# Performance work log

Hardware: AMD Instinct MI355X
Metric: run time of the kernel (lower is better)

Reference implementation:

```python
import jax, jax.numpy as jnp
import numpy as np

N_QUBITS = 8
DIM = 1 << N_QUBITS  # 256
PI = float(np.pi)

# Computational-basis bit signs: s_i = +1 for bit 0, -1 for bit 1 (Z eigenvalues).
# PennyLane convention: wire 0 is the most-significant bit.
_bits = (np.arange(DIM)[:, None] >> (N_QUBITS - 1 - np.arange(N_QUBITS))[None, :]) & 1
SIGNS = jnp.asarray(1.0 - 2.0 * _bits, dtype=jnp.float32)  # [DIM, 8]
PAIR_SIGNS = SIGNS[:, :-1] * SIGNS[:, 1:]                  # [DIM, 7]


def _mlp(x, W1, b1, W2, b2, W3, b3):
    h = jax.nn.relu(x @ W1.T + b1)
    h = jax.nn.relu(h @ W2.T + b2)
    return h @ W3.T + b3


def _embed_state(x):
    """QuantumEmbedding1 (ZZ feature map, IQP-style) on |0>^8.

    H on every wire, RZ(x_i) on wire i, then for i in 0..6:
    CNOT(i,i+1); RZ((pi-x_i)(pi-x_{i+1}), wire i+1); CNOT(i,i+1).
    The whole post-Hadamard circuit is diagonal, so the statevector has
    closed form: psi_b = 2^{-4} exp(-i/2 * phi(b)).
    x: [B, 8] -> psi: [B, 256] complex64.
    """
    single = x @ SIGNS.T                                    # [B, DIM]
    zz = (PI - x[:, :-1]) * (PI - x[:, 1:])                 # [B, 7]
    phase = single + zz @ PAIR_SIGNS.T                      # [B, DIM]
    return jnp.exp(-0.5j * phase) / 16.0                    # complex64


def _mean_rho(psi):
    B = psi.shape[0]
    return jnp.einsum('bi,bj->ij', psi, jnp.conj(psi)) / B  # [256, 256]


def setup_inputs() -> dict:
    key = jax.random.key(0)
    ks = jax.random.split(key, 8)
    B = 65536
    inp = {
        'x1': jax.random.normal(ks[0], (B, 8), dtype=jnp.float32),
        'x0': jax.random.normal(ks[1], (B, 8), dtype=jnp.float32),
        'W1': jax.random.normal(ks[2], (10, 8), dtype=jnp.float32) / np.sqrt(8.0),
        'b1': jnp.zeros((10,), dtype=jnp.float32),
        'W2': jax.random.normal(ks[3], (10, 10), dtype=jnp.float32) / np.sqrt(10.0),
        'b2': jnp.zeros((10,), dtype=jnp.float32),
        'W3': jax.random.normal(ks[4], (8, 10), dtype=jnp.float32) / np.sqrt(10.0),
        'b3': jnp.zeros((8,), dtype=jnp.float32),
    }
    return inp


def reference(x1, x0, W1, b1, W2, b2, W3, b3):
    h1 = _mlp(x1, W1, b1, W2, b2, W3, b3)
    h0 = _mlp(x0, W1, b1, W2, b2, W3, b3)
    rho1 = _mean_rho(_embed_state(h1))
    rho0 = _mean_rho(_embed_state(h0))
    rho_diff = rho1 - rho0
    rho_diff = 0.5 * (rho_diff + jnp.conj(rho_diff.T))  # exact Hermitian
    eigvals = jnp.linalg.eigvalsh(rho_diff)             # real eigenvalues
    return -0.5 * jnp.sum(jnp.abs(eigvals))
```

## Files before the change

kernel.cpp:

```cpp
#include <hip/hip_runtime.h>
#include <cstdint>
#include <cstddef>
#include <utility>

#define PI_F 3.14159265358979323846f

typedef __attribute__((ext_vector_type(8))) _Float16 half8;
typedef __attribute__((ext_vector_type(4))) float f32x4;

struct U4 { unsigned int w[4]; };

static __device__ __forceinline__ unsigned int packhalf2(float c, float s) {
  _Float16 hc = (_Float16)c, hs = (_Float16)s;
  unsigned short uc = __builtin_bit_cast(unsigned short, hc);
  unsigned short us = __builtin_bit_cast(unsigned short, hs);
  return (unsigned int)uc | ((unsigned int)us << 16);
}

__global__ __launch_bounds__(256) void k_mlp(
    const float* __restrict__ x1, const float* __restrict__ x0,
    const float* __restrict__ W1, const float* __restrict__ b1,
    const float* __restrict__ W2, const float* __restrict__ b2,
    const float* __restrict__ W3, const float* __restrict__ b3,
    float* __restrict__ hz, int B, float* __restrict__ scalars,
    float* __restrict__ out) {
  int s = blockIdx.x * blockDim.x + threadIdx.x;
  if (blockIdx.x == 0 && threadIdx.x == 0) {
    scalars[0] = 0.f;
    scalars[1] = 0.f;
    out[0] = 0.f;
  }
  if (s >= 2 * B) return;
  const float* xp = (s < B) ? (x1 + (size_t)s * 8) : (x0 + (size_t)(s - B) * 8);
  float x[8];
#pragma unroll
  for (int k = 0; k < 8; k++) x[k] = xp[k];
  float a1[10];
#pragma unroll
  for (int o = 0; o < 10; o++) {
    float v = b1[o];
#pragma unroll
    for (int k = 0; k < 8; k++) v = fmaf(W1[o * 8 + k], x[k], v);
    a1[o] = fmaxf(v, 0.f);
  }
  float a2[10];
#pragma unroll
  for (int o = 0; o < 10; o++) {
    float v = b2[o];
#pragma unroll
    for (int k = 0; k < 10; k++) v = fmaf(W2[o * 10 + k], a1[k], v);
    a2[o] = fmaxf(v, 0.f);
  }
  float h[8];
#pragma unroll
  for (int o = 0; o < 8; o++) {
    float v = b3[o];
#pragma unroll
    for (int k = 0; k < 10; k++) v = fmaf(W3[o * 10 + k], a2[k], v);
    h[o] = v;
  }
  float outv[16];
#pragma unroll
  for (int k = 0; k < 8; k++) outv[k] = h[k];
#pragma unroll
  for (int k = 0; k < 7; k++) outv[8 + k] = (PI_F - h[k]) * (PI_F - h[k + 1]);
  outv[15] = 0.f;
  float4* dst = (float4*)(hz + (size_t)s * 16);
#pragma unroll
  for (int q = 0; q < 4; q++) dst[q] = ((float4*)outv)[q];
}

__global__ __launch_bounds__(512) void k_gemm_f(const float* __restrict__ hz,
                                                float* __restrict__ P) {
  __shared__ _Float16 lds[2][16384];
  __shared__ float hzb[2][32][17];
  int b = blockIdx.x;
  int qt = (b < 128) ? 0 : (b < 384 ? 1 : 2);
  int z = b - ((qt == 0) ? 0 : (qt == 1) ? 128 : 384);
  int kbPer = (qt == 1) ? 16 : 32;
  int kb0 = z * kbPer;
  int rowLocalBase = (qt == 2) ? 128 : 0;
  int bRowBase = (qt == 1) ? 128 : 0;
  int t = threadIdx.x, wave = t >> 6, lane = t & 63;
  unsigned int reMask = (kb0 < 2048) ? 0u : 0x80008000u;
  unsigned int imMask = (kb0 < 2048) ? 0x80000000u : 0x00008000u;

  int s = t & 31, octH = t >> 5;
  int oct = octH & 7, jHalf = octH >> 3;
  const int nJ = (qt == 1) ? 16 : 8;
  const int jj0 = (qt == 1) ? jHalf * 16 : ((qt == 2) ? 16 : 0) + jHalf * 8;
  const int halfoff = (2 * s) ^ (oct << 3);
  const float S5 = (oct & 4) ? -1.f : 1.f;
  const float S6 = (oct & 2) ? -1.f : 1.f;
  const float S7 = (oct & 1) ? -1.f : 1.f;

  auto loadHz = [&](int kb) {
    if (t < 128) {
      int smp = t >> 2, q = t & 3;
      const float4 v =
          *(const float4*)(hz + (size_t)(kb * 32 + smp) * 16 + q * 4);
      float* d = &hzb[kb & 1][smp][q * 4];
      d[0] = v.x;
      d[1] = v.y;
      d[2] = v.z;
      d[3] = v.w;
    }
  };

  auto gen = [&](int kb, int buf) {
    int hb = kb & 1;
    float h[8], z7[7];
#pragma unroll
    for (int k = 0; k < 8; k++) h[k] = hzb[hb][s][k];
#pragma unroll
    for (int k = 0; k < 7; k++) z7[k] = hzb[hb][s][8 + k];
    int g0 = jj0 ^ (jj0 >> 1);
    float sg[5];
#pragma unroll
    for (int w = 0; w < 5; w++) sg[w] = ((g0 >> (4 - w)) & 1) ? -1.f : 1.f;
    float phi = sg[0] * h[0] + sg[1] * h[1] + sg[2] * h[2] + sg[3] * h[3] +
                sg[4] * h[4] + S5 * h[5] + S6 * h[6] + S7 * h[7] +
                sg[0] * sg[1] * z7[0] + sg[1] * sg[2] * z7[1] +
                sg[2] * sg[3] * z7[2] + sg[3] * sg[4] * z7[3] +
                sg[4] * S5 * z7[4] + S5 * S6 * z7[5] + S6 * S7 * z7[6];
    int g = g0;
    auto emitRow = [&](int gg, float ph) {
      int lr = gg * 8 + oct - rowLocalBase;
      float r = ph * 0.07957747154594767f;
      r = r - floorf(r);
      float sv = __builtin_amdgcn_sinf(r);
      float cv = __builtin_amdgcn_cosf(r);
      *(unsigned int*)&lds[buf][lr * 64 + halfoff] = packhalf2(cv, sv);
    };
    emitRow(g, phi);
#pragma unroll
    for (int stp = 1; stp < 16; stp++) {
      if (stp >= nJ) break;
      const int bbit = __builtin_ctz(stp);
      const int w = 4 - bbit;
      float nbl = (w == 0) ? 0.f : sg[w - 1] * z7[w - 1];
      float nbr = (w == 4) ? S5 * z7[4] : sg[w + 1] * z7[w];
      phi -= 2.f * sg[w] * (h[w] + nbl + nbr);
      sg[w] = -sg[w];
      g ^= (1 << bbit);
      emitRow(g, phi);
    }
  };

  f32x4 accR[2][4] = {};
  f32x4 accI[2][4] = {};

  loadHz(kb0);
  __syncthreads();
  gen(kb0, 0);
  loadHz(kb0 + 1);
  __syncthreads();

  for (int it = 0; it < kbPer; ++it) {
    if (it + 1 < kbPer) {
      gen(kb0 + it + 1, (it + 1) & 1);
      if (it + 2 < kbPer) loadHz(kb0 + it + 2);
    }
    int buf = it & 1;
#pragma unroll
    for (int kk = 0; kk < 2; kk++) {
      int cb = kk * 4 + (lane >> 4);
      half8 af[2];
#pragma unroll
      for (int fr = 0; fr < 2; fr++) {
        int r = (wave >> 1) * 32 + fr * 16 + (lane & 15);
        af[fr] = *(const half8*)&lds[buf][r * 64 + ((cb ^ (r & 7)) << 3)];
      }
#pragma unroll
      for (int fc = 0; fc < 4; fc++) {
        int rb = bRowBase + (wave & 1) * 64 + fc * 16 + (lane & 15);
        half8 bv = *(const half8*)&lds[buf][rb * 64 + ((cb ^ (rb & 7)) << 3)];
        U4 u = __builtin_bit_cast(U4, bv), ur, ui;
#pragma unroll
        for (int q = 0; q < 4; q++) {
          unsigned int xv = u.w[q];
          ur.w[q] = xv ^ reMask;
          ui.w[q] = ((xv << 16) | (xv >> 16)) ^ imMask;
        }
        half8 bfr = __builtin_bit_cast(half8, ur);
        half8 bfi = __builtin_bit_cast(half8, ui);
#pragma unroll
        for (int fr = 0; fr < 2; fr++) {
          accR[fr][fc] = __builtin_amdgcn_mfma_f32_16x16x32_f16(
              af[fr], bfr, accR[fr][fc], 0, 0, 0);
          accI[fr][fc] = __builtin_amdgcn_mfma_f32_16x16x32_f16(
              af[fr], bfi, accI[fr][fc], 0, 0, 0);
        }
      }
    }
    __syncthreads();
  }
  float* PR = P + (size_t)b * 32768;
  float* PI = PR + 16384;
  int r4 = (lane >> 4) * 4, cj = lane & 15;
#pragma unroll
  for (int fr = 0; fr < 2; fr++)
#pragma unroll
    for (int fc = 0; fc < 4; fc++)
#pragma unroll
      for (int r = 0; r < 4; r++) {
        int li = (wave >> 1) * 32 + fr * 16 + r4 + r;
        int lj = (wave & 1) * 64 + fc * 16 + cj;
        PR[li * 128 + lj] = accR[fr][fc][r];
        PI[li * 128 + lj] = accI[fr][fc][r];
      }
}

__global__ __launch_bounds__(128) void k_reduce1(const float* __restrict__ P,
                                                 float* __restrict__ Q) {
  int r = blockIdx.x, qt = blockIdx.y, g = blockIdx.z, c = threadIdx.x;
  int nsl = (qt == 1) ? 32 : 16;
  int b0 = ((qt == 0) ? 0 : (qt == 1) ? 128 : 384) + g * nsl;
  float vR = 0.f, vI = 0.f;
  for (int u = 0; u < nsl; u++) {
    const float* base = P + (size_t)(b0 + u) * 32768 + r * 128 + c;
    vR += base[0];
    vI += base[16384];
  }
  size_t qidx = ((size_t)(g * 3 + qt) * 128 + r) * 128 + c;
  Q[qidx] = vR;
  Q[qidx + (size_t)8 * 3 * 16384] = vI;
}

__global__ __launch_bounds__(128) void k_reduce2(const float* __restrict__ Q,
                                                 float* __restrict__ AR,
                                                 float* __restrict__ AI,
                                                 float* __restrict__ sumsq,
                                                 float scale) {
  int r = blockIdx.x, qt = blockIdx.y, c = threadIdx.x;
  float vR = 0.f, vI = 0.f;
#pragma unroll
  for (int g = 0; g < 8; g++) {
    size_t qidx = ((size_t)(g * 3 + qt) * 128 + r) * 128 + c;
    vR += Q[qidx];
    vI += Q[qidx + (size_t)8 * 3 * 16384];
  }
  vR *= scale;
  vI *= scale;
  int i = (qt == 2) ? 128 + r : r;
  int j = (qt == 0) ? c : 128 + c;
  float ss = 0.f;
  bool diagQ = (qt != 1);
  if (!diagQ || c > r) {
    AR[i * 256 + j] = vR;
    AR[j * 256 + i] = vR;
    AI[i * 256 + j] = vI;
    AI[j * 256 + i] = -vI;
    ss = 2.f * (vR * vR + vI * vI);
  } else if (c == r) {
    AR[i * 256 + j] = vR;
    AI[i * 256 + j] = 0.f;
    ss = vR * vR;
  }
#pragma unroll
  for (int o = 32; o > 0; o >>= 1) ss += __shfl_down(ss, o);
  __shared__ float w2[2];
  if ((c & 63) == 0) w2[c >> 6] = ss;
  __syncthreads();
  if (c == 0) atomicAdd(sumsq, w2[0] + w2[1]);
}

__global__ __launch_bounds__(1024) void k_csq(
    const float* __restrict__ XR, const float* __restrict__ XI,
    float* __restrict__ YR, float* __restrict__ YI,
    float* __restrict__ sumsqY, int accumNorm) {
  __shared__ float rp[16][258][2];
  __shared__ float cpT[16][258][2];
  __shared__ float pacc[3][256][2];
  __shared__ float w16[16];
  int t = threadIdx.x;
  int bi = blockIdx.x >> 4, bj = blockIdx.x & 15;
  {
    int r = t >> 6, c = (t & 63) * 4;
    const float4 vr = *(const float4*)&XR[(bi * 16 + r) * 256 + c];
    const float4 vi = *(const float4*)&XI[(bi * 16 + r) * 256 + c];
    float4 p0 = {vr.x, vi.x, vr.y, vi.y};
    float4 p1 = {vr.z, vi.z, vr.w, vi.w};
    *(float4*)&rp[r][c][0] = p0;
    *(float4*)&rp[r][c + 2][0] = p1;
    int row = t >> 2, c0 = (t & 3) * 4;
    const float4 wr = *(const float4*)&XR[row * 256 + bj * 16 + c0];
    const float4 wi = *(const float4*)&XI[row * 256 + bj * 16 + c0];
    float2 q0 = {wr.x, wi.x}, q1 = {wr.y, wi.y};
    float2 q2 = {wr.z, wi.z}, q3 = {wr.w, wi.w};
    *(float2*)&cpT[c0 + 0][row][0] = q0;
    *(float2*)&cpT[c0 + 1][row][0] = q1;
    *(float2*)&cpT[c0 + 2][row][0] = q2;
    *(float2*)&cpT[c0 + 3][row][0] = q3;
  }
  __syncthreads();
  int sub = t >> 8, tt = t & 255, ty = tt >> 4, tx = tt & 15;
  float sR = 0.f, sI = 0.f;
  int k0 = sub * 64;
#pragma unroll 8
  for (int k = k0; k < k0 + 64; k++) {
    float xr = rp[ty][k][0], xi = rp[ty][k][1];
    float yr = cpT[tx][k][0], yi = cpT[tx][k][1];
    sR = fmaf(xr, yr, sR);
    sR = fmaf(-xi, yi, sR);
    sI = fmaf(xr, yi, sI);
    sI = fmaf(xi, yr, sI);
  }
  if (sub) {
    pacc[sub - 1][tt][0] = sR;
    pacc[sub - 1][tt][1] = sI;
  }
  __syncthreads();
  float v = 0.f;
  if (sub == 0) {
    sR += (pacc[0][tt][0] + pacc[1][tt][0]) + pacc[2][tt][0];
    sI += (pacc[0][tt][1] + pacc[1][tt][1]) + pacc[2][tt][1];
    int i = bi * 16 + ty, j = bj * 16 + tx;
    YR[i * 256 + j] = sR;
    YI[i * 256 + j] = sI;
    if (accumNorm) v = sR * sR + sI * sI;
  }
#pragma unroll
  for (int o = 32; o > 0; o >>= 1) v += __shfl_down(v, o);
  if ((t & 63) == 0) w16[t >> 6] = v;
  __syncthreads();
  if (t == 0 && accumNorm)
    atomicAdd(sumsqY, (w16[0] + w16[1]) + (w16[2] + w16[3]));
}

__global__ __launch_bounds__(1024) void k_cupd(
    const float* __restrict__ XR, const float* __restrict__ XI,
    const float* __restrict__ YR, const float* __restrict__ YI,
    float* __restrict__ ZR, float* __restrict__ ZI,
    const float* __restrict__ scalars, int mode,
    const float* __restrict__ AR, const float* __restrict__ AI,
    float* __restrict__ out, int finalTrace) {
  __shared__ float rp[16][258][2];
  __shared__ float cpT[16][258][2];
  __shared__ float pacc[3][256][2];
  __shared__ float w16[16];
  int t = threadIdx.x;
  int bi = blockIdx.x >> 4, bj = blockIdx.x & 15;
  {
    int r = t >> 6, c = (t & 63) * 4;
    const float4 vr = *(const float4*)&XR[(bi * 16 + r) * 256 + c];
    const float4 vi = *(const float4*)&XI[(bi * 16 + r) * 256 + c];
    float4 p0 = {vr.x, vi.x, vr.y, vi.y};
    float4 p1 = {vr.z, vi.z, vr.w, vi.w};
    *(float4*)&rp[r][c][0] = p0;
    *(float4*)&rp[r][c + 2][0] = p1;
    int row = t >> 2, c0 = (t & 3) * 4;
    const float4 wr = *(const float4*)&YR[row * 256 + bj * 16 + c0];
    const float4 wi = *(const float4*)&YI[row * 256 + bj * 16 + c0];
    float2 q0 = {wr.x, wi.x}, q1 = {wr.y, wi.y};
    float2 q2 = {wr.z, wi.z}, q3 = {wr.w, wi.w};
    *(float2*)&cpT[c0 + 0][row][0] = q0;
    *(float2*)&cpT[c0 + 1][row][0] = q1;
    *(float2*)&cpT[c0 + 2][row][0] = q2;
    *(float2*)&cpT[c0 + 3][row][0] = q3;
  }
  __syncthreads();
  int sub = t >> 8, tt = t & 255, ty = tt >> 4, tx = tt & 15;
  float sR = 0.f, sI = 0.f;
  int k0 = sub * 64;
#pragma unroll 8
  for (int k = k0; k < k0 + 64; k++) {
    float xr = rp[ty][k][0], xi = rp[ty][k][1];
    float yr = cpT[tx][k][0], yi = cpT[tx][k][1];
    sR = fmaf(xr, yr, sR);
    sR = fmaf(-xi, yi, sR);
    sI = fmaf(xr, yi, sI);
    sI = fmaf(xi, yr, sI);
  }
  if (sub) {
    pacc[sub - 1][tt][0] = sR;
    pacc[sub - 1][tt][1] = sI;
  }
  __syncthreads();
  float v = 0.f;
  if (sub == 0) {
    sR += (pacc[0][tt][0] + pacc[1][tt][0]) + pacc[2][tt][0];
    sI += (pacc[0][tt][1] + pacc[1][tt][1]) + pacc[2][tt][1];
    float aC, bC;
    if (mode == 0) {
      float f2 = scalars[0];
      float f = sqrtf(f2);
      float Rhat = 1.41421356f * sqrtf(scalars[1]) / f2;
      float g = 1.0f / (1.75f * Rhat);
      aC = 1.5f * g / f;
      float gf = g / f;
      bC = 0.5f * gf * gf * gf;
    } else if (mode == 1) {
      aC = 2.0f;
      bC = 1.0f;
    } else {
      aC = 1.5f;
      bC = 0.5f;
    }
    int idx = (bi * 16 + ty) * 256 + bj * 16 + tx;
    float zr = aC * XR[idx] - bC * sR;
    float zi = aC * XI[idx] - bC * sI;
    if (!finalTrace) {
      ZR[idx] = zr;
      ZI[idx] = zi;
    } else {
      v = AR[idx] * zr + AI[idx] * zi;
    }
  }
#pragma unroll
  for (int o = 32; o > 0; o >>= 1) v += __shfl_down(v, o);
  if ((t & 63) == 0) w16[t >> 6] = v;
  __syncthreads();
  if (t == 0 && finalTrace)
    atomicAdd(out, -0.5f * ((w16[0] + w16[1]) + (w16[2] + w16[3])));
}

extern "C" void kernel_launch(void* const* d_in, const int* in_sizes, int n_in,
                              void* d_out, int out_size, void* d_ws,
                              size_t ws_size, hipStream_t stream) {
  const float* x1 = (const float*)d_in[0];
  const float* x0 = (const float*)d_in[1];
  const float* W1 = (const float*)d_in[2];
  const float* b1 = (const float*)d_in[3];
  const float* W2 = (const float*)d_in[4];
  const float* b2 = (const float*)d_in[5];
  const float* W3 = (const float*)d_in[6];
  const float* b3 = (const float*)d_in[7];
  (void)n_in;
  (void)out_size;
  (void)ws_size;

  const int B = in_sizes[0] / 8;
  const int total = 2 * B;

  char* ws = (char*)d_ws;
  size_t off = 0;
  auto carve = [&](size_t bytes) -> void* {
    off = (off + 255) & ~(size_t)255;
    void* p = ws + off;
    off += bytes;
    return p;
  };
  float* hz = (float*)carve((size_t)total * 16 * 4);
  float* P = (float*)carve((size_t)512 * 32768 * 4);
  float* Q = (float*)carve((size_t)2 * 8 * 3 * 16384 * 4);
  float* scalars = (float*)carve(256);
  float* AR = (float*)carve(256 * 256 * 4);
  float* AI = (float*)carve(256 * 256 * 4);
  float* XR = (float*)carve(256 * 256 * 4);
  float* XI = (float*)carve(256 * 256 * 4);
  float* YR = (float*)carve(256 * 256 * 4);
  float* YI = (float*)carve(256 * 256 * 4);
  float* ZR = (float*)carve(256 * 256 * 4);
  float* ZI = (float*)carve(256 * 256 * 4);

  k_mlp<<<(total + 255) / 256, 256, 0, stream>>>(
      x1, x0, W1, b1, W2, b2, W3, b3, hz, B, scalars, (float*)d_out);
  k_gemm_f<<<512, 512, 0, stream>>>(hz, P);
  k_reduce1<<<dim3(128, 3, 8), 128, 0, stream>>>(P, Q);
  k_reduce2<<<dim3(128, 3), 128, 0, stream>>>(Q, AR, AI, scalars,
                                              1.0f / (256.0f * (float)B));

  const int NIT = 11;
  float *cR = AR, *cI = AI, *nR = XR, *nI = XI;
  for (int it = 0; it < NIT; it++) {
    int mode = (it == 0) ? 0 : (it <= 6 ? 1 : 2);
    int fin = (it == NIT - 1) ? 1 : 0;
    k_csq<<<256, 1024, 0, stream>>>(cR, cI, YR, YI, scalars + 1, it == 0);
    k_cupd<<<256, 1024, 0, stream>>>(cR, cI, YR, YI, nR, nI, scalars, mode, AR,
                                     AI, (float*)d_out, fin);
    if (it == 0) {
      cR = XR; cI = XI; nR = ZR; nI = ZI;
    } else {
      std::swap(cR, nR);
      std::swap(cI, nI);
    }
  }
}
```

Measured before the change: 219.1 us.

## Exploit Hermitian symmetry in Newton-Schulz iterations and interleave phase generation with MFMA

The matrix-squaring and update kernels now compute only the lower-triangular 16x16 tiles (136 blocks instead of 256) and mirror each result into the transposed tile as its conjugate. Norm and trace sums double-weight the off-diagonal tiles to compensate. Separately, the GEMM kernel splits the phase-generation loop into two halves interleaved with the two MFMA k-steps, using s_setprio to favour the matrix work, and makes the generation count a compile-time constant. The symmetry trick assumes every iterate stays exactly Hermitian, and the mirrored stores are strided and uncoalesced.

Result: slower. 261.8 us (+19.5%).

```diff
diff --git a/kernel.cpp b/kernel.cpp
--- a/kernel.cpp
+++ b/kernel.cpp
@@ -2,6 +2,7 @@
 #include <cstdint>
 #include <cstddef>
 #include <utility>
+#include <type_traits>
 
 #define PI_F 3.14159265358979323846f
 
@@ -87,8 +88,6 @@
 
   int s = t & 31, octH = t >> 5;
   int oct = octH & 7, jHalf = octH >> 3;
-  const int nJ = (qt == 1) ? 16 : 8;
-  const int jj0 = (qt == 1) ? jHalf * 16 : ((qt == 2) ? 16 : 0) + jHalf * 8;
   const int halfoff = (2 * s) ^ (oct << 3);
   const float S5 = (oct & 4) ? -1.f : 1.f;
   const float S6 = (oct & 2) ? -1.f : 1.f;
@@ -107,94 +106,130 @@
     }
   };
 
-  auto gen = [&](int kb, int buf) {
-    int hb = kb & 1;
-    float h[8], z7[7];
-#pragma unroll
-    for (int k = 0; k < 8; k++) h[k] = hzb[hb][s][k];
-#pragma unroll
-    for (int k = 0; k < 7; k++) z7[k] = hzb[hb][s][8 + k];
-    int g0 = jj0 ^ (jj0 >> 1);
-    float sg[5];
-#pragma unroll
-    for (int w = 0; w < 5; w++) sg[w] = ((g0 >> (4 - w)) & 1) ? -1.f : 1.f;
-    float phi = sg[0] * h[0] + sg[1] * h[1] + sg[2] * h[2] + sg[3] * h[3] +
-                sg[4] * h[4] + S5 * h[5] + S6 * h[6] + S7 * h[7] +
-                sg[0] * sg[1] * z7[0] + sg[1] * sg[2] * z7[1] +
-                sg[2] * sg[3] * z7[2] + sg[3] * sg[4] * z7[3] +
-                sg[4] * S5 * z7[4] + S5 * S6 * z7[5] + S6 * S7 * z7[6];
-    int g = g0;
-    auto emitRow = [&](int gg, float ph) {
-      int lr = gg * 8 + oct - rowLocalBase;
-      float r = ph * 0.07957747154594767f;
+  f32x4 accR[2][4] = {};
+  f32x4 accI[2][4] = {};
+
+  auto mfmaKK = [&](int kk, int buf) {
+    int cb = kk * 4 + (lane >> 4);
+    half8 af[2];
+#pragma unroll
+    for (int fr = 0; fr < 2; fr++) {
+      int r = (wave >> 1) * 32 + fr * 16 + (lane & 15);
+      af[fr] = *(const half8*)&lds[buf][r * 64 + ((cb ^ (r & 7)) << 3)];
+    }
+#pragma unroll
+    for (int fc = 0; fc < 4; fc++) {
+      int rb = bRowBase + (wave & 1) * 64 + fc * 16 + (lane & 15);
+      half8 bv = *(const half8*)&lds[buf][rb * 64 + ((cb ^ (rb & 7)) << 3)];
+      U4 u = __builtin_bit_cast(U4, bv), ur, ui;
+#pragma unroll
+      for (int q = 0; q < 4; q++) {
+        unsigned int xv = u.w[q];
+        ur.w[q] = xv ^ reMask;
+        ui.w[q] = ((xv << 16) | (xv >> 16)) ^ imMask;
+      }
+      half8 bfr = __builtin_bit_cast(half8, ur);
+      half8 bfi = __builtin_bit_cast(half8, ui);
+#pragma unroll
+      for (int fr = 0; fr < 2; fr++) {
+        accR[fr][fc] = __builtin_amdgcn_mfma_f32_16x16x32_f16(
+            af[fr], bfr, accR[fr][fc], 0, 0, 0);
+        accI[fr][fc] = __builtin_amdgcn_mfma_f32_16x16x32_f16(
+            af[fr], bfi, accI[fr][fc], 0, 0, 0);
+      }
+    }
+  };
+
+  auto runLoop = [&](auto njc) {
+    constexpr int NJ = decltype(njc)::value;
+    constexpr int NH = NJ / 2;
+    const int jj0 = (NJ == 16) ? jHalf * 16
+                               : ((qt == 2) ? 16 : 0) + jHalf * 8;
+    float h[8], z7[7], sg[5], phi;
+    int g;
+    auto initGen = [&](int kb) {
+      int hb = kb & 1;
+#pragma unroll
+      for (int k = 0; k < 8; k++) h[k] = hzb[hb][s][k];
+#pragma unroll
+      for (int k = 0; k < 7; k++) z7[k] = hzb[hb][s][8 + k];
+      int g0 = jj0 ^ (jj0 >> 1);
+#pragma unroll
+      for (int w = 0; w < 5; w++) sg[w] = ((g0 >> (4 - w)) & 1) ? -1.f : 1.f;
+      phi = sg[0] * h[0] + sg[1] * h[1] + sg[2] * h[2] + sg[3] * h[3] +
+            sg[4] * h[4] + S5 * h[5] + S6 * h[6] + S7 * h[7] +
+            sg[0] * sg[1] * z7[0] + sg[1] * sg[2] * z7[1] +
+            sg[2] * sg[3] * z7[2] + sg[3] * sg[4] * z7[3] +
+            sg[4] * S5 * z7[4] + S5 * S6 * z7[5] + S6 * S7 * z7[6];
+      g = g0;
+    };
+    auto emitRow = [&](int buf) {
+      int lr = g * 8 + oct - rowLocalBase;
+      float r = phi * 0.07957747154594767f;
       r = r - floorf(r);
       float sv = __builtin_amdgcn_sinf(r);
       float cv = __builtin_amdgcn_cosf(r);
       *(unsigned int*)&lds[buf][lr * 64 + halfoff] = packhalf2(cv, sv);
     };
-    emitRow(g, phi);
-#pragma unroll
-    for (int stp = 1; stp < 16; stp++) {
-      if (stp >= nJ) break;
-      const int bbit = __builtin_ctz(stp);
-      const int w = 4 - bbit;
-      float nbl = (w == 0) ? 0.f : sg[w - 1] * z7[w - 1];
-      float nbr = (w == 4) ? S5 * z7[4] : sg[w + 1] * z7[w];
-      phi -= 2.f * sg[w] * (h[w] + nbl + nbr);
-      sg[w] = -sg[w];
-      g ^= (1 << bbit);
-      emitRow(g, phi);
+#define GSTEP(stp)                                             \
+  {                                                            \
+    const int bbit = __builtin_ctz(stp);                       \
+    const int w = 4 - bbit;                                    \
+    float nbl = (w == 0) ? 0.f : sg[w - 1] * z7[w - 1];        \
+    float nbr = (w == 4) ? S5 * z7[4] : sg[w + 1] * z7[w];     \
+    phi -= 2.f * sg[w] * (h[w] + nbl + nbr);                   \
+    sg[w] = -sg[w];                                            \
+    g ^= (1 << bbit);                                          \
+  }
+    auto genA = [&](int buf) {
+      emitRow(buf);
+#pragma unroll
+      for (int stp = 1; stp < NH; stp++) {
+        GSTEP(stp);
+        emitRow(buf);
+      }
+    };
+    auto genB = [&](int buf) {
+#pragma unroll
+      for (int stp = NH; stp < NJ; stp++) {
+        GSTEP(stp);
+        emitRow(buf);
+      }
+    };
+#undef GSTEP
+
+    loadHz(kb0);
+    __syncthreads();
+    initGen(kb0);
+    genA(0);
+    genB(0);
+    loadHz(kb0 + 1);
+    __syncthreads();
+
+    for (int it = 0; it < kbPer; ++it) {
+      int buf = it & 1, nb = buf ^ 1;
+      bool hasNext = (it + 1 < kbPer);
+      if (hasNext) initGen(kb0 + it + 1);
+      __builtin_amdgcn_s_setprio(1);
+      mfmaKK(0, buf);
+      __builtin_amdgcn_s_setprio(0);
+      if (hasNext) genA(nb);
+      __builtin_amdgcn_s_setprio(1);
+      mfmaKK(1, buf);
+      __builtin_amdgcn_s_setprio(0);
+      if (hasNext) {
+        genB(nb);
+        if (it + 2 < kbPer) loadHz(kb0 + it + 2);
+      }
+      __syncthreads();
     }
   };
 
-  f32x4 accR[2][4] = {};
-  f32x4 accI[2][4] = {};
-
-  loadHz(kb0);
-  __syncthreads();
-  gen(kb0, 0);
-  loadHz(kb0 + 1);
-  __syncthreads();
-
-  for (int it = 0; it < kbPer; ++it) {
-    if (it + 1 < kbPer) {
-      gen(kb0 + it + 1, (it + 1) & 1);
-      if (it + 2 < kbPer) loadHz(kb0 + it + 2);
-    }
-    int buf = it & 1;
-#pragma unroll
-    for (int kk = 0; kk < 2; kk++) {
-      int cb = kk * 4 + (lane >> 4);
-      half8 af[2];
-#pragma unroll
-      for (int fr = 0; fr < 2; fr++) {
-        int r = (wave >> 1) * 32 + fr * 16 + (lane & 15);
-        af[fr] = *(const half8*)&lds[buf][r * 64 + ((cb ^ (r & 7)) << 3)];
-      }
-#pragma unroll
-      for (int fc = 0; fc < 4; fc++) {
-        int rb = bRowBase + (wave & 1) * 64 + fc * 16 + (lane & 15);
-        half8 bv = *(const half8*)&lds[buf][rb * 64 + ((cb ^ (rb & 7)) << 3)];
-        U4 u = __builtin_bit_cast(U4, bv), ur, ui;
-#pragma unroll
-        for (int q = 0; q < 4; q++) {
-          unsigned int xv = u.w[q];
-          ur.w[q] = xv ^ reMask;
-          ui.w[q] = ((xv << 16) | (xv >> 16)) ^ imMask;
-        }
-        half8 bfr = __builtin_bit_cast(half8, ur);
-        half8 bfi = __builtin_bit_cast(half8, ui);
-#pragma unroll
-        for (int fr = 0; fr < 2; fr++) {
-          accR[fr][fc] = __builtin_amdgcn_mfma_f32_16x16x32_f16(
-              af[fr], bfr, accR[fr][fc], 0, 0, 0);
-          accI[fr][fc] = __builtin_amdgcn_mfma_f32_16x16x32_f16(
-              af[fr], bfi, accI[fr][fc], 0, 0, 0);
-        }
-      }
-    }
-    __syncthreads();
-  }
+  if (qt == 1)
+    runLoop(std::integral_constant<int, 16>{});
+  else
+    runLoop(std::integral_constant<int, 8>{});
+
   float* PR = P + (size_t)b * 32768;
   float* PI = PR + 16384;
   int r4 = (lane >> 4) * 4, cj = lane & 15;
@@ -265,6 +300,13 @@
   if (c == 0) atomicAdd(sumsq, w2[0] + w2[1]);
 }
 
+static __device__ __forceinline__ void unrank(int k, int& bi, int& bj) {
+  bi = (int)((sqrtf(8.f * (float)k + 1.f) - 1.f) * 0.5f);
+  if ((bi + 1) * (bi + 2) / 2 <= k) bi++;
+  if (bi * (bi + 1) / 2 > k) bi--;
+  bj = k - bi * (bi + 1) / 2;
+}
+
 __global__ __launch_bounds__(1024) void k_csq(
     const float* __restrict__ XR, const float* __restrict__ XI,
     float* __restrict__ YR, float* __restrict__ YI,
@@ -274,7 +316,8 @@
   __shared__ float pacc[3][256][2];
   __shared__ float w16[16];
   int t = threadIdx.x;
-  int bi = blockIdx.x >> 4, bj = blockIdx.x & 15;
+  int bi, bj;
+  unrank(blockIdx.x, bi, bj);
   {
     int r = t >> 6, c = (t & 63) * 4;
     const float4 vr = *(const float4*)&XR[(bi * 16 + r) * 256 + c];
@@ -318,7 +361,14 @@
     int i = bi * 16 + ty, j = bj * 16 + tx;
     YR[i * 256 + j] = sR;
     YI[i * 256 + j] = sI;
-    if (accumNorm) v = sR * sR + sI * sI;
+    if (bi != bj) {
+      YR[j * 256 + i] = sR;
+      YI[j * 256 + i] = -sI;
+    }
+    if (accumNorm) {
+      float wgt = (bi == bj) ? 1.f : 2.f;
+      v = wgt * (sR * sR + sI * sI);
+    }
   }
 #pragma unroll
   for (int o = 32; o > 0; o >>= 1) v += __shfl_down(v, o);
@@ -340,7 +390,8 @@
   __shared__ float pacc[3][256][2];
   __shared__ float w16[16];
   int t = threadIdx.x;
-  int bi = blockIdx.x >> 4, bj = blockIdx.x & 15;
+  int bi, bj;
+  unrank(blockIdx.x, bi, bj);
   {
     int r = t >> 6, c = (t & 63) * 4;
     const float4 vr = *(const float4*)&XR[(bi * 16 + r) * 256 + c];
@@ -403,8 +454,13 @@
     if (!finalTrace) {
       ZR[idx] = zr;
       ZI[idx] = zi;
+      if (bi != bj) {
+        ZR[(bj * 16 + tx) * 256 + bi * 16 + ty] = zr;
+        ZI[(bj * 16 + tx) * 256 + bi * 16 + ty] = -zi;
+      }
     } else {
-      v = AR[idx] * zr + AI[idx] * zi;
+      float wgt = (bi == bj) ? 1.f : 2.f;
+      v = wgt * (AR[idx] * zr + AI[idx] * zi);
     }
   }
 #pragma unroll
@@ -466,8 +522,8 @@
   for (int it = 0; it < NIT; it++) {
     int mode = (it == 0) ? 0 : (it <= 6 ? 1 : 2);
     int fin = (it == NIT - 1) ? 1 : 0;
-    k_csq<<<256, 1024, 0, stream>>>(cR, cI, YR, YI, scalars + 1, it == 0);
-    k_cupd<<<256, 1024, 0, stream>>>(cR, cI, YR, YI, nR, nI, scalars, mode, AR,
+    k_csq<<<136, 1024, 0, stream>>>(cR, cI, YR, YI, scalars + 1, it == 0);
+    k_cupd<<<136, 1024, 0, stream>>>(cR, cI, YR, YI, nR, nI, scalars, mode, AR,
                                      AI, (float*)d_out, fin);
     if (it == 0) {
       cR = XR; cI = XI; nR = ZR; nI = ZI;
```
